# Kernel optimization log

Measured on AMD Instinct MI355X. Metric: run time of the kernel, lower is better.

Reference implementation:

```python
import jax, jax.numpy as jnp
import numpy as np

IN, H, T = 16, 64, 25

def _lstm_layer(x, w_ih, w_hh, b_ih, b_hh):
    # x: [B,T,I]; w_ih: [4H,I]; w_hh: [4H,H]; biases: [4H]
    B = x.shape[0]
    x_proj = jnp.einsum('bti,gi->btg', x, w_ih) + b_ih + b_hh  # [B,T,4H]
    h0 = jnp.zeros((B, H), x.dtype)
    c0 = jnp.zeros((B, H), x.dtype)
    def step(carry, xt):
        h, c = carry
        gates = xt + h @ w_hh.T  # [B,4H]
        i, f, g, o = jnp.split(gates, 4, axis=-1)  # torch gate order i,f,g,o
        i = jax.nn.sigmoid(i); f = jax.nn.sigmoid(f)
        g = jnp.tanh(g);       o = jax.nn.sigmoid(o)
        c = f * c + i * g
        h = o * jnp.tanh(c)
        return (h, c), h
    _, hs = jax.lax.scan(step, (h0, c0), jnp.swapaxes(x_proj, 0, 1))  # [T,B,H]
    return jnp.swapaxes(hs, 0, 1)  # [B,T,H]


def setup_inputs() -> dict:
    key = jax.random.key(0)
    ks = jax.random.split(key, 20)
    s = 1.0 / np.sqrt(H)
    u = lambda k, shp: jax.random.uniform(k, shp, jnp.float32, -s, s)
    inp = {
        'x': jax.random.normal(ks[0], (32768, T, IN), jnp.float32),
        'w_ih0': u(ks[1], (4 * H, IN)), 'w_hh0': u(ks[2], (4 * H, H)),
        'b_ih0': u(ks[3], (4 * H,)),    'b_hh0': u(ks[4], (4 * H,)),
        'w_ih1': u(ks[5], (4 * H, H)),  'w_hh1': u(ks[6], (4 * H, H)),
        'b_ih1': u(ks[7], (4 * H,)),    'b_hh1': u(ks[8], (4 * H,)),
        'fc1_w': u(ks[9],  (128, H * T)), 'fc1_b': u(ks[10], (128,)),
        'fc2_w': u(ks[11], (128, H * T)), 'fc2_b': u(ks[12], (128,)),
        'fc3_w': u(ks[13], (128, H * T)), 'fc3_b': u(ks[14], (128,)),
        'l1_w': u(ks[15], (5, 128)),  'l1_b': u(ks[16], (5,)),
        'l2_w': u(ks[17], (4, 128)),  'l2_b': u(ks[18], (4,)),
        'l3_w': u(ks[19], (8, 128)),  'l3_b': jnp.zeros((8,), jnp.float32),
    }
    return inp


def reference(x, w_ih0, w_hh0, b_ih0, b_hh0, w_ih1, w_hh1, b_ih1, b_hh1,
              fc1_w, fc1_b, fc2_w, fc2_b, fc3_w, fc3_b,
              l1_w, l1_b, l2_w, l2_b, l3_w, l3_b):
    out = _lstm_layer(x, w_ih0, w_hh0, b_ih0, b_hh0)
    out = _lstm_layer(out, w_ih1, w_hh1, b_ih1, b_hh1)  # [B,T,H]
    flat = out.reshape(out.shape[0], -1)  # [B, T*H]
    x1 = jax.nn.relu(flat @ fc1_w.T + fc1_b)
    x2 = jax.nn.relu(flat @ fc2_w.T + fc2_b)
    x3 = jax.nn.relu(flat @ fc3_w.T + fc3_b)
    o1 = x1 @ l1_w.T + l1_b
    o2 = x2 @ l2_w.T + l2_b
    o3 = x3 @ l3_w.T + l3_b
    return (o1, o2, o3)
```

## Files before the change

### kernel.cpp

```cpp
#include <hip/hip_runtime.h>
#include <stdint.h>

#define BATCH 32768
#define TT    25

typedef float f32x4 __attribute__((ext_vector_type(4)));
typedef short s16x8 __attribute__((ext_vector_type(8)));

__device__ __align__(16) short g_Wc[384 * 1600];

#define LOG2E 1.442695040888963f

__device__ __forceinline__ uint32_t f2bf(float v){
  uint32_t u = __float_as_uint(v);
  return (u + 0x7fffu + ((u >> 16) & 1u)) >> 16;
}
__device__ __forceinline__ short f2bfs(float v){ return (short)f2bf(v); }

__device__ __forceinline__ float sigm(float x){
  float e = __builtin_amdgcn_exp2f(-LOG2E * x);
  return __builtin_amdgcn_rcpf(1.0f + e);
}
__device__ __forceinline__ float tanh_(float x){
  float e = __builtin_amdgcn_exp2f(-2.0f*LOG2E * x);
  return 2.0f*__builtin_amdgcn_rcpf(1.0f + e) - 1.0f;
}
__device__ __forceinline__ s16x8 pack8(float4 a, float4 b){
  s16x8 v;
  v[0]=f2bfs(a.x); v[1]=f2bfs(a.y); v[2]=f2bfs(a.z); v[3]=f2bfs(a.w);
  v[4]=f2bfs(b.x); v[5]=f2bfs(b.y); v[6]=f2bfs(b.z); v[7]=f2bfs(b.w);
  return v;
}

__global__ void conv_wc_kernel(const float* __restrict__ fc1w,
                               const float* __restrict__ fc2w,
                               const float* __restrict__ fc3w){
  const int j = blockIdx.x;
  const float* src = (j < 128) ? fc1w + j*1600
                   : (j < 256) ? fc2w + (j-128)*1600
                               : fc3w + (j-256)*1600;
  for (int k = threadIdx.x; k < 1600; k += 256)
    g_Wc[j*1600 + k] = f2bfs(src[k]);
}

__global__ __launch_bounds__(512, 1) void lstm2_mfma_kernel(
    const float* __restrict__ x,
    const float* __restrict__ wih0, const float* __restrict__ whh0,
    const float* __restrict__ bih0, const float* __restrict__ bhh0,
    const float* __restrict__ wih1, const float* __restrict__ whh1,
    const float* __restrict__ bih1, const float* __restrict__ bhh1,
    short* __restrict__ flat)
{
  __shared__ short Abuf[4*64*64];
  char* const Ab = (char*)Abuf;

  const int tid  = threadIdx.x;
  const int lane = tid & 63;
  const int wv   = tid >> 6;
  const int w4   = wv & 3;
  const int wg   = wv >> 2;
  const int lrow = lane & 15;
  const int lk   = lane >> 4;
  const int sw   = (lrow & 7) << 4;
  const int sb   = blockIdx.x * 64;
  const int u    = w4*16 + lrow;

  {
    s16x8 z = {0,0,0,0,0,0,0,0};
    int idx = tid * 32;
    char* pz = Ab + ((idx < 8192) ? 8192 + idx : 16384 + idx);
    *(s16x8*)pz = z; *(s16x8*)(pz + 16) = z;
  }

  s16x8 W1f[4][4], B0x[4], B0h[4][2];
  #pragma unroll
  for (int n = 0; n < 4; n++){
    const int g = n*64 + u;
    #pragma unroll
    for (int kt = 0; kt < 4; kt++){
      const float* src = (kt < 2 ? wih1 + g*64 + kt*32 : whh1 + g*64 + (kt-2)*32) + lk*8;
      W1f[n][kt] = pack8(*(const float4*)src, *(const float4*)(src+4));
    }
    if (lk < 2){
      const float* src = wih0 + g*16 + lk*8;
      B0x[n] = pack8(*(const float4*)src, *(const float4*)(src+4));
    } else {
      s16x8 z = {0,0,0,0,0,0,0,0}; B0x[n] = z;
    }
    #pragma unroll
    for (int kt = 0; kt < 2; kt++){
      const float* src = whh0 + g*64 + kt*32 + lk*8;
      B0h[n][kt] = pack8(*(const float4*)src, *(const float4*)(src+4));
    }
  }

  float b0v[4], b1v[4];
  #pragma unroll
  for (int n = 0; n < 4; n++){
    b0v[n] = bih0[n*64+u] + bhh0[n*64+u];
    b1v[n] = bih1[n*64+u] + bhh1[n*64+u];
  }

  const float* xbase[2];
  #pragma unroll
  for (int m = 0; m < 2; m++)
    xbase[m] = x + (size_t)(sb + wg*32 + m*16 + lrow)*(TT*16) + (lk&1)*8;
  s16x8 xf[2];
  #pragma unroll
  for (int m = 0; m < 2; m++)
    xf[m] = pack8(*(const float4*)(xbase[m]), *(const float4*)(xbase[m] + 4));

  float c0[2][4], c1[2][4];
  #pragma unroll
  for (int m = 0; m < 2; m++)
    #pragma unroll
    for (int r = 0; r < 4; r++){ c0[m][r] = 0.f; c1[m][r] = 0.f; }

  __syncthreads();

  #pragma unroll 1
  for (int t = 0; t < TT; t++){
    const int p  = t & 1;
    const int pn = p ^ 1;
    f32x4 acc[2][4];
    #pragma unroll
    for (int m = 0; m < 2; m++)
      #pragma unroll
      for (int n = 0; n < 4; n++){ f32x4 iv = {b0v[n],b0v[n],b0v[n],b0v[n]}; acc[m][n] = iv; }
    #pragma unroll
    for (int m = 0; m < 2; m++)
      #pragma unroll
      for (int n = 0; n < 4; n++)
        acc[m][n] = __builtin_amdgcn_mfma_f32_16x16x32_bf16(xf[m], B0x[n], acc[m][n], 0, 0, 0);
    #pragma unroll
    for (int kt = 0; kt < 2; kt++){
      s16x8 a[2];
      #pragma unroll
      for (int m = 0; m < 2; m++){
        int row = wg*32 + m*16 + lrow;
        a[m] = *(const s16x8*)(Ab + pn*8192 + row*128 + ((kt*64 + lk*16) ^ sw));
      }
      #pragma unroll
      for (int m = 0; m < 2; m++)
        #pragma unroll
        for (int n = 0; n < 4; n++)
          acc[m][n] = __builtin_amdgcn_mfma_f32_16x16x32_bf16(a[m], B0h[n][kt], acc[m][n], 0, 0, 0);
    }
    short hb[2][4];
    #pragma unroll
    for (int m = 0; m < 2; m++)
      #pragma unroll
      for (int r = 0; r < 4; r++){
        float iv = sigm(acc[m][0][r]);
        float fv = sigm(acc[m][1][r]);
        float gv = tanh_(acc[m][2][r]);
        float ov = sigm(acc[m][3][r]);
        float c  = fmaf(fv, c0[m][r], iv*gv); c0[m][r] = c;
        hb[m][r] = f2bfs(ov * tanh_(c));
      }
    #pragma unroll
    for (int m = 0; m < 2; m++)
      #pragma unroll
      for (int r = 0; r < 4; r++){
        int mine = (int)(uint16_t)hb[m][r];
        int part = __shfl_xor(mine, 1);
        if ((lane & 1) == 0){
          int s_ = wg*32 + m*16 + lk*4 + r;
          uint32_t pk = (uint32_t)mine | ((uint32_t)part << 16);
          *(uint32_t*)(Ab + p*8192 + s_*128 + ((u*2) ^ ((s_&7)<<4))) = pk;
        }
      }
    __syncthreads();

    s16x8 xfn[2];
    if (t + 1 < TT){
      #pragma unroll
      for (int m = 0; m < 2; m++)
        xfn[m] = pack8(*(const float4*)(xbase[m] + (t+1)*16),
                       *(const float4*)(xbase[m] + (t+1)*16 + 4));
    }
    #pragma unroll
    for (int m = 0; m < 2; m++)
      #pragma unroll
      for (int n = 0; n < 4; n++){ f32x4 iv = {b1v[n],b1v[n],b1v[n],b1v[n]}; acc[m][n] = iv; }
    #pragma unroll
    for (int kt = 0; kt < 4; kt++){
      const int reg = (kt < 2) ? p*8192 : 16384 + pn*8192;
      const int ko  = (kt & 1) * 64;
      s16x8 a[2];
      #pragma unroll
      for (int m = 0; m < 2; m++){
        int row = wg*32 + m*16 + lrow;
        a[m] = *(const s16x8*)(Ab + reg + row*128 + ((ko + lk*16) ^ sw));
      }
      #pragma unroll
      for (int m = 0; m < 2; m++)
        #pragma unroll
        for (int n = 0; n < 4; n++)
          acc[m][n] = __builtin_amdgcn_mfma_f32_16x16x32_bf16(a[m], W1f[n][kt], acc[m][n], 0, 0, 0);
    }
    #pragma unroll
    for (int m = 0; m < 2; m++)
      #pragma unroll
      for (int r = 0; r < 4; r++){
        float iv = sigm(acc[m][0][r]);
        float fv = sigm(acc[m][1][r]);
        float gv = tanh_(acc[m][2][r]);
        float ov = sigm(acc[m][3][r]);
        float c  = fmaf(fv, c1[m][r], iv*gv); c1[m][r] = c;
        hb[m][r] = f2bfs(ov * tanh_(c));
      }
    #pragma unroll
    for (int m = 0; m < 2; m++)
      #pragma unroll
      for (int r = 0; r < 4; r++){
        int mine = (int)(uint16_t)hb[m][r];
        int part = __shfl_xor(mine, 1);
        if ((lane & 1) == 0){
          int s_ = wg*32 + m*16 + lk*4 + r;
          uint32_t pk = (uint32_t)mine | ((uint32_t)part << 16);
          *(uint32_t*)(Ab + 16384 + p*8192 + s_*128 + ((u*2) ^ ((s_&7)<<4))) = pk;
          *(uint32_t*)(flat + (size_t)(sb+s_)*1600 + t*64 + u) = pk;
        }
      }
    __syncthreads();
    #pragma unroll
    for (int m = 0; m < 2; m++) xf[m] = xfn[m];
  }
}

__global__ __launch_bounds__(512,1) void fc_mfma_kernel(
    const short* __restrict__ flat,
    const float* __restrict__ fc1b, const float* __restrict__ fc2b, const float* __restrict__ fc3b,
    const float* __restrict__ l1w,  const float* __restrict__ l1b,
    const float* __restrict__ l2w,  const float* __restrict__ l2b,
    const float* __restrict__ l3w,  const float* __restrict__ l3b,
    float* __restrict__ out)
{
  __shared__ float R[64*388];
  const int tid  = threadIdx.x;
  const int lane = tid & 63;
  const int wv   = tid >> 6;
  const int w4   = wv >> 1;
  const int wg   = wv & 1;
  const int lrow = lane & 15;
  const int lk   = lane >> 4;
  const int sb   = blockIdx.x * 64;

  f32x4 acc[2][6];
  #pragma unroll
  for (int n = 0; n < 6; n++){
    int j = w4*96 + n*16 + lrow;
    float bv = (j < 128) ? fc1b[j] : (j < 256) ? fc2b[j-128] : fc3b[j-256];
    #pragma unroll
    for (int m = 0; m < 2; m++){ f32x4 iv = {bv,bv,bv,bv}; acc[m][n] = iv; }
  }

  const char* Abase = (const char*)(flat + (size_t)sb*1600);
  const char* Bbase = (const char*)g_Wc;
  #pragma unroll 1
  for (int kc = 0; kc < 50; kc++){
    s16x8 a[2], b[6];
    #pragma unroll
    for (int m = 0; m < 2; m++)
      a[m] = *(const s16x8*)(Abase + (size_t)(wg*32 + m*16 + lrow)*3200 + kc*64 + lk*16);
    #pragma unroll
    for (int n = 0; n < 6; n++)
      b[n] = *(const s16x8*)(Bbase + (size_t)(w4*96 + n*16 + lrow)*3200 + kc*64 + lk*16);
    #pragma unroll
    for (int m = 0; m < 2; m++)
      #pragma unroll
      for (int n = 0; n < 6; n++)
        acc[m][n] = __builtin_amdgcn_mfma_f32_16x16x32_bf16(a[m], b[n], acc[m][n], 0, 0, 0);
  }

  #pragma unroll
  for (int m = 0; m < 2; m++)
    #pragma unroll
    for (int n = 0; n < 6; n++)
      #pragma unroll
      for (int r = 0; r < 4; r++){
        int s_ = wg*32 + m*16 + lk*4 + r;
        int fc = w4*96 + n*16 + lrow;
        R[s_*388 + fc] = fmaxf(acc[m][n][r], 0.f);
      }
  __syncthreads();

  const int s    = tid & 63;
  const int gsel = tid >> 6;
  #pragma unroll
  for (int qi = 0; qi < 3; qi++){
    int q = gsel + qi*8;
    if (q >= 17) break;
    const float* wp; float bb; int rbase; float* op;
    if (q < 5)      { wp = l1w + q*128;     bb = l1b[q];   rbase = 0;
                      op = out + (size_t)(sb+s)*5 + q; }
    else if (q < 9) { int q2 = q-5; wp = l2w + q2*128; bb = l2b[q2]; rbase = 128;
                      op = out + (size_t)BATCH*5 + (size_t)(sb+s)*4 + q2; }
    else            { int q3 = q-9; wp = l3w + q3*128; bb = l3b[q3]; rbase = 256;
                      op = out + (size_t)BATCH*9 + (size_t)(sb+s)*8 + q3; }
    float o = bb;
    const float* Rr = &R[s*388 + rbase];
    #pragma unroll
    for (int k = 0; k < 128; k += 4){
      float4 rv = *(const float4*)(Rr + k);
      o += rv.x*wp[k] + rv.y*wp[k+1] + rv.z*wp[k+2] + rv.w*wp[k+3];
    }
    *op = o;
  }
}

extern "C" void kernel_launch(void* const* d_in, const int* in_sizes, int n_in,
                              void* d_out, int out_size, void* d_ws, size_t ws_size,
                              hipStream_t stream)
{
  const float* x    = (const float*)d_in[0];
  const float* wih0 = (const float*)d_in[1];
  const float* whh0 = (const float*)d_in[2];
  const float* bih0 = (const float*)d_in[3];
  const float* bhh0 = (const float*)d_in[4];
  const float* wih1 = (const float*)d_in[5];
  const float* whh1 = (const float*)d_in[6];
  const float* bih1 = (const float*)d_in[7];
  const float* bhh1 = (const float*)d_in[8];
  const float* fc1w = (const float*)d_in[9];
  const float* fc1b = (const float*)d_in[10];
  const float* fc2w = (const float*)d_in[11];
  const float* fc2b = (const float*)d_in[12];
  const float* fc3w = (const float*)d_in[13];
  const float* fc3b = (const float*)d_in[14];
  const float* l1w  = (const float*)d_in[15];
  const float* l1b  = (const float*)d_in[16];
  const float* l2w  = (const float*)d_in[17];
  const float* l2b  = (const float*)d_in[18];
  const float* l3w  = (const float*)d_in[19];
  const float* l3b  = (const float*)d_in[20];

  float* out  = (float*)d_out;
  short* flat = (short*)d_ws;
  if (ws_size < (size_t)BATCH*1600*2) return;

  conv_wc_kernel<<<dim3(384), dim3(256), 0, stream>>>(fc1w, fc2w, fc3w);

  lstm2_mfma_kernel<<<dim3(BATCH/64), dim3(512), 0, stream>>>(
      x, wih0, whh0, bih0, bhh0, wih1, whh1, bih1, bhh1, flat);

  fc_mfma_kernel<<<dim3(BATCH/64), dim3(512), 0, stream>>>(
      flat, fc1b, fc2b, fc3b, l1w, l1b, l2w, l2b, l3w, l3b, out);
}
```

Before: 445.2 us.

## Shrink LSTM blocks, pack bf16 via hardware cvt, and run head layers on MFMA

The LSTM kernel moves from 64 samples per 512-thread block to 32 samples per 256-thread block, giving twice as many blocks and halving the shared buffers. Float-to-bf16 packing now uses the v_cvt_pk_bf16_f32 instruction instead of manual rounding, and the shuffle is done on floats. The FC kernel now has each of 4 waves cover all 64 rows with 96 output columns, which changes how flat rows are reused. It also stores the ReLU output as swizzled bf16 in LDS and computes the small output heads with MFMA instead of scalar dot products. This trades some precision in the head layers (bf16 activations and weights) for fewer ALU instructions and better occupancy.

```diff
diff --git a/kernel.cpp b/kernel.cpp
--- a/kernel.cpp
+++ b/kernel.cpp
@@ -17,6 +17,12 @@
 }
 __device__ __forceinline__ short f2bfs(float v){ return (short)f2bf(v); }
 
+__device__ __forceinline__ uint32_t cvt_pk_bf16(float lo, float hi){
+  uint32_t d;
+  asm("v_cvt_pk_bf16_f32 %0, %1, %2" : "=v"(d) : "v"(lo), "v"(hi));
+  return d;
+}
+
 __device__ __forceinline__ float sigm(float x){
   float e = __builtin_amdgcn_exp2f(-LOG2E * x);
   return __builtin_amdgcn_rcpf(1.0f + e);
@@ -26,10 +32,12 @@
   return 2.0f*__builtin_amdgcn_rcpf(1.0f + e) - 1.0f;
 }
 __device__ __forceinline__ s16x8 pack8(float4 a, float4 b){
-  s16x8 v;
-  v[0]=f2bfs(a.x); v[1]=f2bfs(a.y); v[2]=f2bfs(a.z); v[3]=f2bfs(a.w);
-  v[4]=f2bfs(b.x); v[5]=f2bfs(b.y); v[6]=f2bfs(b.z); v[7]=f2bfs(b.w);
-  return v;
+  union { uint32_t w[4]; s16x8 v; } u_;
+  u_.w[0] = cvt_pk_bf16(a.x, a.y);
+  u_.w[1] = cvt_pk_bf16(a.z, a.w);
+  u_.w[2] = cvt_pk_bf16(b.x, b.y);
+  u_.w[3] = cvt_pk_bf16(b.z, b.w);
+  return u_.v;
 }
 
 __global__ void conv_wc_kernel(const float* __restrict__ fc1w,
@@ -43,7 +51,7 @@
     g_Wc[j*1600 + k] = f2bfs(src[k]);
 }
 
-__global__ __launch_bounds__(512, 1) void lstm2_mfma_kernel(
+__global__ __launch_bounds__(256, 1) void lstm2_mfma_kernel(
     const float* __restrict__ x,
     const float* __restrict__ wih0, const float* __restrict__ whh0,
     const float* __restrict__ bih0, const float* __restrict__ bhh0,
@@ -51,24 +59,22 @@
     const float* __restrict__ bih1, const float* __restrict__ bhh1,
     short* __restrict__ flat)
 {
-  __shared__ short Abuf[4*64*64];
+  __shared__ short Abuf[4*32*64];
   char* const Ab = (char*)Abuf;
 
   const int tid  = threadIdx.x;
   const int lane = tid & 63;
-  const int wv   = tid >> 6;
-  const int w4   = wv & 3;
-  const int wg   = wv >> 2;
+  const int w4   = tid >> 6;
   const int lrow = lane & 15;
   const int lk   = lane >> 4;
   const int sw   = (lrow & 7) << 4;
-  const int sb   = blockIdx.x * 64;
+  const int sb   = blockIdx.x * 32;
   const int u    = w4*16 + lrow;
 
   {
     s16x8 z = {0,0,0,0,0,0,0,0};
     int idx = tid * 32;
-    char* pz = Ab + ((idx < 8192) ? 8192 + idx : 16384 + idx);
+    char* pz = Ab + ((idx < 4096) ? 4096 + idx : 8192 + idx);
     *(s16x8*)pz = z; *(s16x8*)(pz + 16) = z;
   }
 
@@ -104,7 +110,7 @@
   const float* xbase[2];
   #pragma unroll
   for (int m = 0; m < 2; m++)
-    xbase[m] = x + (size_t)(sb + wg*32 + m*16 + lrow)*(TT*16) + (lk&1)*8;
+    xbase[m] = x + (size_t)(sb + m*16 + lrow)*(TT*16) + (lk&1)*8;
   s16x8 xf[2];
   #pragma unroll
   for (int m = 0; m < 2; m++)
@@ -137,8 +143,8 @@
       s16x8 a[2];
       #pragma unroll
       for (int m = 0; m < 2; m++){
-        int row = wg*32 + m*16 + lrow;
-        a[m] = *(const s16x8*)(Ab + pn*8192 + row*128 + ((kt*64 + lk*16) ^ sw));
+        int row = m*16 + lrow;
+        a[m] = *(const s16x8*)(Ab + pn*4096 + row*128 + ((kt*64 + lk*16) ^ sw));
       }
       #pragma unroll
       for (int m = 0; m < 2; m++)
@@ -146,7 +152,6 @@
         for (int n = 0; n < 4; n++)
           acc[m][n] = __builtin_amdgcn_mfma_f32_16x16x32_bf16(a[m], B0h[n][kt], acc[m][n], 0, 0, 0);
     }
-    short hb[2][4];
     #pragma unroll
     for (int m = 0; m < 2; m++)
       #pragma unroll
@@ -156,18 +161,12 @@
         float gv = tanh_(acc[m][2][r]);
         float ov = sigm(acc[m][3][r]);
         float c  = fmaf(fv, c0[m][r], iv*gv); c0[m][r] = c;
-        hb[m][r] = f2bfs(ov * tanh_(c));
-      }
-    #pragma unroll
-    for (int m = 0; m < 2; m++)
-      #pragma unroll
-      for (int r = 0; r < 4; r++){
-        int mine = (int)(uint16_t)hb[m][r];
-        int part = __shfl_xor(mine, 1);
+        float hv = ov * tanh_(c);
+        float hp = __shfl_xor(hv, 1);
+        uint32_t pk = cvt_pk_bf16(hv, hp);
         if ((lane & 1) == 0){
-          int s_ = wg*32 + m*16 + lk*4 + r;
-          uint32_t pk = (uint32_t)mine | ((uint32_t)part << 16);
-          *(uint32_t*)(Ab + p*8192 + s_*128 + ((u*2) ^ ((s_&7)<<4))) = pk;
+          int s_ = m*16 + lk*4 + r;
+          *(uint32_t*)(Ab + p*4096 + s_*128 + ((u*2) ^ ((s_&7)<<4))) = pk;
         }
       }
     __syncthreads();
@@ -185,12 +184,12 @@
       for (int n = 0; n < 4; n++){ f32x4 iv = {b1v[n],b1v[n],b1v[n],b1v[n]}; acc[m][n] = iv; }
     #pragma unroll
     for (int kt = 0; kt < 4; kt++){
-      const int reg = (kt < 2) ? p*8192 : 16384 + pn*8192;
+      const int reg = (kt < 2) ? p*4096 : 8192 + pn*4096;
       const int ko  = (kt & 1) * 64;
       s16x8 a[2];
       #pragma unroll
       for (int m = 0; m < 2; m++){
-        int row = wg*32 + m*16 + lrow;
+        int row = m*16 + lrow;
         a[m] = *(const s16x8*)(Ab + reg + row*128 + ((ko + lk*16) ^ sw));
       }
       #pragma unroll
@@ -208,18 +207,12 @@
         float gv = tanh_(acc[m][2][r]);
         float ov = sigm(acc[m][3][r]);
         float c  = fmaf(fv, c1[m][r], iv*gv); c1[m][r] = c;
-        hb[m][r] = f2bfs(ov * tanh_(c));
-      }
-    #pragma unroll
-    for (int m = 0; m < 2; m++)
-      #pragma unroll
-      for (int r = 0; r < 4; r++){
-        int mine = (int)(uint16_t)hb[m][r];
-        int part = __shfl_xor(mine, 1);
+        float hv = ov * tanh_(c);
+        float hp = __shfl_xor(hv, 1);
+        uint32_t pk = cvt_pk_bf16(hv, hp);
         if ((lane & 1) == 0){
-          int s_ = wg*32 + m*16 + lk*4 + r;
-          uint32_t pk = (uint32_t)mine | ((uint32_t)part << 16);
-          *(uint32_t*)(Ab + 16384 + p*8192 + s_*128 + ((u*2) ^ ((s_&7)<<4))) = pk;
+          int s_ = m*16 + lk*4 + r;
+          *(uint32_t*)(Ab + 8192 + p*4096 + s_*128 + ((u*2) ^ ((s_&7)<<4))) = pk;
           *(uint32_t*)(flat + (size_t)(sb+s_)*1600 + t*64 + u) = pk;
         }
       }
@@ -229,7 +222,7 @@
   }
 }
 
-__global__ __launch_bounds__(512,1) void fc_mfma_kernel(
+__global__ __launch_bounds__(256,1) void fc_mfma_kernel(
     const short* __restrict__ flat,
     const float* __restrict__ fc1b, const float* __restrict__ fc2b, const float* __restrict__ fc3b,
     const float* __restrict__ l1w,  const float* __restrict__ l1b,
@@ -237,77 +230,110 @@
     const float* __restrict__ l3w,  const float* __restrict__ l3b,
     float* __restrict__ out)
 {
-  __shared__ float R[64*388];
+  __shared__ short Rs[64*384];
+  char* const Rb = (char*)Rs;
   const int tid  = threadIdx.x;
   const int lane = tid & 63;
   const int wv   = tid >> 6;
-  const int w4   = wv >> 1;
-  const int wg   = wv & 1;
   const int lrow = lane & 15;
   const int lk   = lane >> 4;
   const int sb   = blockIdx.x * 64;
 
-  f32x4 acc[2][6];
+  f32x4 acc[4][6];
   #pragma unroll
   for (int n = 0; n < 6; n++){
-    int j = w4*96 + n*16 + lrow;
+    int j = wv*96 + n*16 + lrow;
     float bv = (j < 128) ? fc1b[j] : (j < 256) ? fc2b[j-128] : fc3b[j-256];
     #pragma unroll
-    for (int m = 0; m < 2; m++){ f32x4 iv = {bv,bv,bv,bv}; acc[m][n] = iv; }
+    for (int m = 0; m < 4; m++){ f32x4 iv = {bv,bv,bv,bv}; acc[m][n] = iv; }
   }
 
   const char* Abase = (const char*)(flat + (size_t)sb*1600);
   const char* Bbase = (const char*)g_Wc;
   #pragma unroll 1
   for (int kc = 0; kc < 50; kc++){
-    s16x8 a[2], b[6];
-    #pragma unroll
-    for (int m = 0; m < 2; m++)
-      a[m] = *(const s16x8*)(Abase + (size_t)(wg*32 + m*16 + lrow)*3200 + kc*64 + lk*16);
+    s16x8 a[4], b[6];
+    #pragma unroll
+    for (int m = 0; m < 4; m++)
+      a[m] = *(const s16x8*)(Abase + (size_t)(m*16+lrow)*3200 + kc*64 + lk*16);
     #pragma unroll
     for (int n = 0; n < 6; n++)
-      b[n] = *(const s16x8*)(Bbase + (size_t)(w4*96 + n*16 + lrow)*3200 + kc*64 + lk*16);
-    #pragma unroll
-    for (int m = 0; m < 2; m++)
+      b[n] = *(const s16x8*)(Bbase + (size_t)(wv*96+n*16+lrow)*3200 + kc*64 + lk*16);
+    #pragma unroll
+    for (int m = 0; m < 4; m++)
       #pragma unroll
       for (int n = 0; n < 6; n++)
         acc[m][n] = __builtin_amdgcn_mfma_f32_16x16x32_bf16(a[m], b[n], acc[m][n], 0, 0, 0);
   }
 
   #pragma unroll
-  for (int m = 0; m < 2; m++)
+  for (int m = 0; m < 4; m++)
     #pragma unroll
     for (int n = 0; n < 6; n++)
       #pragma unroll
       for (int r = 0; r < 4; r++){
-        int s_ = wg*32 + m*16 + lk*4 + r;
-        int fc = w4*96 + n*16 + lrow;
-        R[s_*388 + fc] = fmaxf(acc[m][n][r], 0.f);
+        float v  = fmaxf(acc[m][n][r], 0.f);
+        float vp = __shfl_xor(v, 1);
+        uint32_t pk = cvt_pk_bf16(v, vp);
+        if ((lane & 1) == 0){
+          int s_ = m*16 + lk*4 + r;
+          int fc = wv*96 + n*16 + lrow;
+          *(uint32_t*)(Rb + s_*768 + ((fc*2) ^ ((s_&7)<<4))) = pk;
+        }
       }
   __syncthreads();
 
-  const int s    = tid & 63;
-  const int gsel = tid >> 6;
-  #pragma unroll
-  for (int qi = 0; qi < 3; qi++){
-    int q = gsel + qi*8;
-    if (q >= 17) break;
-    const float* wp; float bb; int rbase; float* op;
-    if (q < 5)      { wp = l1w + q*128;     bb = l1b[q];   rbase = 0;
-                      op = out + (size_t)(sb+s)*5 + q; }
-    else if (q < 9) { int q2 = q-5; wp = l2w + q2*128; bb = l2b[q2]; rbase = 128;
-                      op = out + (size_t)BATCH*5 + (size_t)(sb+s)*4 + q2; }
-    else            { int q3 = q-9; wp = l3w + q3*128; bb = l3b[q3]; rbase = 256;
-                      op = out + (size_t)BATCH*9 + (size_t)(sb+s)*8 + q3; }
-    float o = bb;
-    const float* Rr = &R[s*388 + rbase];
-    #pragma unroll
-    for (int k = 0; k < 128; k += 4){
-      float4 rv = *(const float4*)(Rr + k);
-      o += rv.x*wp[k] + rv.y*wp[k+1] + rv.z*wp[k+2] + rv.w*wp[k+3];
-    }
-    *op = o;
-  }
+  const float* Lw[3] = {l1w, l2w, l3w};
+  const int   odim[3] = {5, 4, 8};
+  s16x8 Bh[3][4];
+  #pragma unroll
+  for (int q = 0; q < 3; q++){
+    #pragma unroll
+    for (int kt = 0; kt < 4; kt++){
+      if (lrow < odim[q]){
+        const float* src = Lw[q] + lrow*128 + kt*32 + lk*8;
+        Bh[q][kt] = pack8(*(const float4*)src, *(const float4*)(src+4));
+      } else {
+        s16x8 z = {0,0,0,0,0,0,0,0}; Bh[q][kt] = z;
+      }
+    }
+  }
+  f32x4 acc2[4][3];
+  {
+    float bv0 = (lrow < 5) ? l1b[lrow] : 0.f;
+    float bv1 = (lrow < 4) ? l2b[lrow] : 0.f;
+    float bv2 = (lrow < 8) ? l3b[lrow] : 0.f;
+    #pragma unroll
+    for (int m = 0; m < 4; m++){
+      f32x4 i0 = {bv0,bv0,bv0,bv0}; acc2[m][0] = i0;
+      f32x4 i1 = {bv1,bv1,bv1,bv1}; acc2[m][1] = i1;
+      f32x4 i2 = {bv2,bv2,bv2,bv2}; acc2[m][2] = i2;
+    }
+  }
+  #pragma unroll
+  for (int q = 0; q < 3; q++){
+    #pragma unroll
+    for (int kt = 0; kt < 4; kt++){
+      s16x8 a[4];
+      #pragma unroll
+      for (int m = 0; m < 4; m++){
+        int row = m*16 + lrow;
+        a[m] = *(const s16x8*)(Rb + row*768 + ((q*256 + kt*64 + lk*16) ^ ((row&7)<<4)));
+      }
+      #pragma unroll
+      for (int m = 0; m < 4; m++)
+        acc2[m][q] = __builtin_amdgcn_mfma_f32_16x16x32_bf16(a[m], Bh[q][kt], acc2[m][q], 0, 0, 0);
+    }
+  }
+  #pragma unroll
+  for (int m = 0; m < 4; m++)
+    #pragma unroll
+    for (int r = 0; r < 4; r++){
+      int smp = sb + m*16 + lk*4 + r;
+      if (lrow < 5) out[(size_t)smp*5 + lrow] = acc2[m][0][r];
+      if (lrow < 4) out[(size_t)BATCH*5 + (size_t)smp*4 + lrow] = acc2[m][1][r];
+      if (lrow < 8) out[(size_t)BATCH*9 + (size_t)smp*8 + lrow] = acc2[m][2][r];
+    }
 }
 
 extern "C" void kernel_launch(void* const* d_in, const int* in_sizes, int n_in,
@@ -342,9 +368,9 @@
 
   conv_wc_kernel<<<dim3(384), dim3(256), 0, stream>>>(fc1w, fc2w, fc3w);
 
-  lstm2_mfma_kernel<<<dim3(BATCH/64), dim3(512), 0, stream>>>(
+  lstm2_mfma_kernel<<<dim3(BATCH/32), dim3(256), 0, stream>>>(
       x, wih0, whh0, bih0, bhh0, wih1, whh1, bih1, bhh1, flat);
 
-  fc_mfma_kernel<<<dim3(BATCH/64), dim3(512), 0, stream>>>(
+  fc_mfma_kernel<<<dim3(BATCH/64), dim3(256), 0, stream>>>(
       flat, fc1b, fc2b, fc3b, l1w, l1b, l2w, l2b, l3w, l3b, out);
 }
```

New measurement: 470.3 us. 1.06x slower.
